# Kernel optimization log

Hardware: AMD Instinct MI355X
Metric: run time of the kernel (lower is better)

Reference implementation:

```python
import jax, jax.numpy as jnp
import numpy as np

HEADS = 16
DIM_HEAD = 64
SCALE = DIM_HEAD ** -0.5
LN_EPS = 1e-5


def setup_inputs() -> dict:
    key = jax.random.key(0)
    k1, k2, k3 = jax.random.split(key, 3)
    b, s, d = 2, 2048, 1024
    inner = HEADS * DIM_HEAD
    x = jax.random.normal(k1, (b, s, d), dtype=jnp.float32)
    w_qkv = jax.random.normal(k2, (d, 3 * inner), dtype=jnp.float32) * (d ** -0.5)
    w_out = jax.random.normal(k3, (inner, d), dtype=jnp.float32) * (inner ** -0.5)
    return {
        "x": x,
        "ln_gamma": jnp.ones((d,), jnp.float32),
        "ln_beta": jnp.zeros((d,), jnp.float32),
        "w_qkv": w_qkv,
        "w_out": w_out,
        "b_out": jnp.zeros((d,), jnp.float32),
    }


def _layernorm(x, gamma, beta):
    mu = jnp.mean(x, axis=-1, keepdims=True)
    var = jnp.var(x, axis=-1, keepdims=True)
    return (x - mu) * jax.lax.rsqrt(var + LN_EPS) * gamma + beta


def reference(x, ln_gamma, ln_beta, w_qkv, w_out, b_out):
    b, s, d = x.shape
    xn = _layernorm(x, ln_gamma, ln_beta)
    qkv = xn @ w_qkv                       # [b, s, 3*inner]
    q, k, v = jnp.split(qkv, 3, axis=-1)
    def heads(t):
        return t.reshape(b, s, HEADS, DIM_HEAD).transpose(0, 2, 1, 3)  # [b, h, s, dh]
    q, k, v = heads(q), heads(k), heads(v)
    dots = jnp.einsum("bhqd,bhkd->bhqk", q, k) * SCALE   # [b, h, s, s]
    attn = jax.nn.softmax(dots, axis=-1)
    out = jnp.einsum("bhqk,bhkd->bhqd", attn, v)          # [b, h, s, dh]
    out = out.transpose(0, 2, 1, 3).reshape(b, s, HEADS * DIM_HEAD)
    return out @ w_out + b_out
```

## Files before the change

kernel.cpp:

```cpp
#include <hip/hip_runtime.h>
#include <hip/hip_bf16.h>
#include <stdint.h>

#define NH     16
#define DHEAD  64
#define SEQ    2048
#define DMODEL 1024
#define NBATCH 2
#define INNER  1024
#define QKVN   3072
#define ROWS   4096
#define ATT_QB 64
#define ATT_KB 64

typedef __attribute__((ext_vector_type(8))) __bf16 bf16x8;
typedef __attribute__((ext_vector_type(4))) float floatx4;
typedef __attribute__((ext_vector_type(16))) float floatx16;

__device__ __forceinline__ unsigned short f2bf(float f) {
    union { __bf16 b; unsigned short u; } c; c.b = (__bf16)f; return c.u;
}

__device__ __forceinline__ unsigned int pk2(float lo, float hi) {
    union { ushort2 s; unsigned int u; } c;
    c.s.x = f2bf(lo); c.s.y = f2bf(hi); return c.u;
}

__device__ __forceinline__ float fexp2(float x) {
#if __has_builtin(__builtin_amdgcn_exp2f)
    return __builtin_amdgcn_exp2f(x);
#else
    float r; asm("v_exp_f32 %0, %1" : "=v"(r) : "v"(x)); return r;
#endif
}

typedef __attribute__((address_space(1))) void gvoid;
typedef __attribute__((address_space(3))) void lvoid;
__device__ __forceinline__ void gl_lds16(const void* g, void* l) {
    __builtin_amdgcn_global_load_lds((gvoid*)g, (lvoid*)l, 16, 0, 0);
}

__global__ __launch_bounds__(256) void prep_kernel(
        const float* __restrict__ x,
        const float* __restrict__ gamma,
        const float* __restrict__ beta,
        unsigned short* __restrict__ xn,
        const float* __restrict__ wqkv, unsigned short* __restrict__ wqkvT,
        const float* __restrict__ wout, unsigned short* __restrict__ woutT) {
    __shared__ unsigned short tile[32][33];
    __shared__ float red[4][2];
    const int t = threadIdx.x;
    if (blockIdx.z == 2) {
        const int row = blockIdx.y * 128 + blockIdx.x;
        const size_t base = (size_t)row * DMODEL + t * 4;
        float4 v = *(const float4*)(x + base);
        float s  = v.x + v.y + v.z + v.w;
        float ss = v.x*v.x + v.y*v.y + v.z*v.z + v.w*v.w;
        for (int off = 32; off >= 1; off >>= 1) {
            s  += __shfl_xor(s,  off);
            ss += __shfl_xor(ss, off);
        }
        const int w = t >> 6, lane = t & 63;
        if (lane == 0) { red[w][0] = s; red[w][1] = ss; }
        __syncthreads();
        if (t == 0) {
            float S  = red[0][0] + red[1][0] + red[2][0] + red[3][0];
            float SS = red[0][1] + red[1][1] + red[2][1] + red[3][1];
            float mu  = S * (1.f / DMODEL);
            float var = SS * (1.f / DMODEL) - mu * mu;
            red[0][0] = mu; red[0][1] = rsqrtf(var + 1e-5f);
        }
        __syncthreads();
        const float mu = red[0][0], rstd = red[0][1];
        float4 g = *(const float4*)(gamma + t * 4);
        float4 bb = *(const float4*)(beta + t * 4);
        ushort4 o;
        o.x = f2bf((v.x - mu) * rstd * g.x + bb.x);
        o.y = f2bf((v.y - mu) * rstd * g.y + bb.y);
        o.z = f2bf((v.z - mu) * rstd * g.z + bb.z);
        o.w = f2bf((v.w - mu) * rstd * g.w + bb.w);
        *(ushort4*)(xn + base) = o;
        return;
    }
    const float* in; unsigned short* out; int rows, cols;
    if (blockIdx.z == 0) {
        if (blockIdx.x >= QKVN / 32) return;
        in = wqkv; out = wqkvT; rows = DMODEL; cols = QKVN;
    } else {
        if (blockIdx.x >= DMODEL / 32) return;
        in = wout; out = woutT; rows = INNER; cols = DMODEL;
    }
    const int bx = blockIdx.x * 32, by = blockIdx.y * 32;
    const int tx = t & 31, ty = t >> 5;
    for (int i = ty; i < 32; i += 8)
        tile[i][tx] = f2bf(in[(size_t)(by + i) * cols + bx + tx]);
    __syncthreads();
    for (int i = ty; i < 32; i += 8)
        out[(size_t)(bx + i) * rows + by + tx] = tile[tx][i];
}

__global__ __launch_bounds__(256) void gemm_qkv(
        const unsigned short* __restrict__ A,
        const unsigned short* __restrict__ Bt,
        unsigned short* __restrict__ qP,
        unsigned short* __restrict__ kP,
        unsigned short* __restrict__ vT) {
    const int K = DMODEL;
    __shared__ __align__(16) unsigned short smem[3 * 8192];
    const int t = threadIdx.x;
    const int mBase = blockIdx.y * 128, nBase = blockIdx.x * 128;
    const int w = t >> 6, lane = t & 63, quad = lane >> 4, l16 = lane & 15;
    const int wm = (w >> 1) * 64, wn = (w & 1) * 64;
    const int srow = t >> 2, sch = t & 3;
    floatx4 acc[4][4];
    for (int mi = 0; mi < 4; mi++)
        for (int ni = 0; ni < 4; ni++) acc[mi][ni] = (floatx4)0.f;

    auto stage = [&](int k0, int bi) {
        unsigned short* sA = smem + bi * 8192;
        unsigned short* sB = sA + 4096;
        #pragma unroll
        for (int c = 0; c < 2; c++) {
            const int row = c * 64 + srow;
            const int gcol = (sch ^ ((row >> 1) & 3)) * 8;
            gl_lds16(&A[(size_t)(mBase + row) * K + k0 + gcol], &sA[(c * 256 + w * 64) * 8]);
            gl_lds16(&Bt[(size_t)(nBase + row) * K + k0 + gcol], &sB[(c * 256 + w * 64) * 8]);
        }
    };

    const int NK = K / 32;
    stage(0, 0);
    stage(32, 1);
    for (int kk = 0; kk < NK; ++kk) {
        if (kk + 1 < NK) { asm volatile("s_waitcnt vmcnt(4)" ::: "memory"); }
        else             { asm volatile("s_waitcnt vmcnt(0)" ::: "memory"); }
        __builtin_amdgcn_sched_barrier(0);
        __builtin_amdgcn_s_barrier();
        const unsigned short* sA = smem + (kk % 3) * 8192;
        const unsigned short* sB = sA + 4096;
        bf16x8 af[4], bfv[4];
        #pragma unroll
        for (int mi = 0; mi < 4; mi++) {
            const int r = wm + mi * 16 + l16;
            af[mi] = *(const bf16x8*)&sA[r * 32 + (quad ^ ((r >> 1) & 3)) * 8];
        }
        #pragma unroll
        for (int ni = 0; ni < 4; ni++) {
            const int r = wn + ni * 16 + l16;
            bfv[ni] = *(const bf16x8*)&sB[r * 32 + (quad ^ ((r >> 1) & 3)) * 8];
        }
        if (kk + 2 < NK) stage((kk + 2) * 32, (kk + 2) % 3);
        __builtin_amdgcn_s_setprio(1);
        #pragma unroll
        for (int mi = 0; mi < 4; mi++)
            #pragma unroll
            for (int ni = 0; ni < 4; ni++)
                acc[mi][ni] = __builtin_amdgcn_mfma_f32_16x16x32_bf16(
                    af[mi], bfv[ni], acc[mi][ni], 0, 0, 0);
        __builtin_amdgcn_s_setprio(0);
    }
    __syncthreads();
    const int reg = nBase >> 10;
    if (reg == 2) {
        #pragma unroll
        for (int ni = 0; ni < 4; ni++) {
            const int col = nBase + wn + ni * 16 + l16;
            const int h = (col & 1023) >> 6, dh = col & 63;
            #pragma unroll
            for (int mi = 0; mi < 4; mi++) {
                const int row0 = mBase + wm + mi * 16 + quad * 4;
                const int b = row0 >> 11, s0 = row0 & 2047;
                ushort4 o;
                o.x = f2bf(acc[mi][ni][0]); o.y = f2bf(acc[mi][ni][1]);
                o.z = f2bf(acc[mi][ni][2]); o.w = f2bf(acc[mi][ni][3]);
                *(ushort4*)&vT[((size_t)(b * NH + h) * DHEAD + dh) * SEQ + s0] = o;
            }
        }
    } else {
        unsigned short* dst = (reg == 0) ? qP : kP;
        const float scl = (reg == 0) ? 0.18033688011112042f : 1.f;
        const int hh = ((nBase + wn) & 1023) >> 6;
        unsigned short* tb_ = smem + w * (64 * 72);
        #pragma unroll
        for (int mi = 0; mi < 4; mi++)
            #pragma unroll
            for (int ni = 0; ni < 4; ni++)
                #pragma unroll
                for (int i = 0; i < 4; i++)
                    tb_[(mi * 16 + quad * 4 + i) * 72 + ni * 16 + l16] =
                        f2bf(acc[mi][ni][i] * scl);
        asm volatile("s_waitcnt lgkmcnt(0)" ::: "memory");
        const int row_g = mBase + wm + lane;
        const int b = row_g >> 11, sr = row_g & 2047;
        unsigned short* orow = dst + ((size_t)(b * NH + hh) * SEQ + sr) * DHEAD;
        #pragma unroll
        for (int c = 0; c < 8; c++)
            *(bf16x8*)&orow[c * 8] = *(const bf16x8*)&tb_[lane * 72 + c * 8];
    }
}

__global__ __launch_bounds__(256) void gemm_out(
        const unsigned short* __restrict__ A,
        const unsigned short* __restrict__ Bt,
        float* __restrict__ C,
        const int M, const int N, const int K,
        const float* __restrict__ bias) {
    __shared__ __align__(16) unsigned short smem[3 * 6144];
    const int t = threadIdx.x;
    const int mBase = blockIdx.y * 128, nBase = blockIdx.x * 64;
    const int w = t >> 6, lane = t & 63, quad = lane >> 4, l16 = lane & 15;
    const int wm = (w >> 1) * 64, wn = (w & 1) * 32;
    const int srow = t >> 2, sch = t & 3;
    floatx4 acc[4][2];
    for (int mi = 0; mi < 4; mi++)
        for (int ni = 0; ni < 2; ni++) acc[mi][ni] = (floatx4)0.f;

    auto stage = [&](int k0, int bi) {
        unsigned short* sA = smem + bi * 6144;
        unsigned short* sB = sA + 4096;
        #pragma unroll
        for (int c = 0; c < 2; c++) {
            const int row = c * 64 + srow;
            const int gcol = (sch ^ ((row >> 1) & 3)) * 8;
            gl_lds16(&A[(size_t)(mBase + row) * K + k0 + gcol], &sA[(c * 256 + w * 64) * 8]);
        }
        {
            const int gcol = (sch ^ ((srow >> 1) & 3)) * 8;
            gl_lds16(&Bt[(size_t)(nBase + srow) * K + k0 + gcol], &sB[(w * 64) * 8]);
        }
    };

    const int NK = K / 32;
    stage(0, 0);
    stage(32, 1);
    for (int kk = 0; kk < NK; ++kk) {
        if (kk + 1 < NK) { asm volatile("s_waitcnt vmcnt(3)" ::: "memory"); }
        else             { asm volatile("s_waitcnt vmcnt(0)" ::: "memory"); }
        __builtin_amdgcn_sched_barrier(0);
        __builtin_amdgcn_s_barrier();
        const unsigned short* sA = smem + (kk % 3) * 6144;
        const unsigned short* sB = sA + 4096;
        bf16x8 af[4], bfv[2];
        #pragma unroll
        for (int mi = 0; mi < 4; mi++) {
            const int r = wm + mi * 16 + l16;
            af[mi] = *(const bf16x8*)&sA[r * 32 + (quad ^ ((r >> 1) & 3)) * 8];
        }
        #pragma unroll
        for (int ni = 0; ni < 2; ni++) {
            const int r = wn + ni * 16 + l16;
            bfv[ni] = *(const bf16x8*)&sB[r * 32 + (quad ^ ((r >> 1) & 3)) * 8];
        }
        if (kk + 2 < NK) stage((kk + 2) * 32, (kk + 2) % 3);
        __builtin_amdgcn_s_setprio(1);
        #pragma unroll
        for (int mi = 0; mi < 4; mi++)
            #pragma unroll
            for (int ni = 0; ni < 2; ni++)
                acc[mi][ni] = __builtin_amdgcn_mfma_f32_16x16x32_bf16(
                    af[mi], bfv[ni], acc[mi][ni], 0, 0, 0);
        __builtin_amdgcn_s_setprio(0);
    }
    #pragma unroll
    for (int mi = 0; mi < 4; mi++)
        #pragma unroll
        for (int ni = 0; ni < 2; ni++) {
            const int col = nBase + wn + ni * 16 + l16;
            const float badd = bias ? bias[col] : 0.f;
            #pragma unroll
            for (int i = 0; i < 4; i++) {
                const int row = mBase + wm + mi * 16 + quad * 4 + i;
                C[(size_t)row * N + col] = acc[mi][ni][i] + badd;
            }
        }
}

__global__ __launch_bounds__(256, 4) void attn_kernel(
        const unsigned short* __restrict__ qP,
        const unsigned short* __restrict__ kP,
        const unsigned short* __restrict__ vT,
        unsigned short* __restrict__ aout) {
    __shared__ __align__(16) unsigned short sK[2][ATT_KB * 64];
    __shared__ __align__(16) unsigned short sV[2][ATT_KB * 64];
    const int t = threadIdx.x, w = t >> 6, lane = t & 63;
    const int l32 = lane & 31, half = lane >> 5;
    const int qh = w & 1, kh = w >> 1;
    const int bid = blockIdx.x;
    const int xcd = bid & 7, slot = bid >> 3;
    const int bh = xcd * 4 + (slot >> 5);
    const int qb = slot & 31;
    const int b = bh >> 4, h = bh & 15;
    const int qbase = qb * ATT_QB + qh * 32;

    bf16x8 qf[4];
    #pragma unroll
    for (int kd = 0; kd < 4; kd++)
        qf[kd] = *(const bf16x8*)&qP[
            ((size_t)bh * SEQ + qbase + l32) * DHEAD + kd * 16 + half * 8];

    floatx16 oac[2];
    oac[0] = (floatx16)0.f; oac[1] = (floatx16)0.f;
    float lS = 0.f;

    const unsigned short* kb = kP + (size_t)bh * SEQ * DHEAD;
    const unsigned short* vb = vT + (size_t)bh * DHEAD * SEQ;
    const int r8 = lane >> 3, sw8 = ((lane & 7) ^ r8) * 8;

    auto stage = [&](int it, int bi) {
        const int kv0 = it * ATT_KB;
        #pragma unroll
        for (int ii = 0; ii < 2; ii++) {
            const int row = w * 16 + ii * 8 + r8;
            gl_lds16(kb + (size_t)(kv0 + row) * DHEAD + sw8,
                     (void*)&sK[bi][(w * 16 + ii * 8) * 64]);
            gl_lds16(vb + (size_t)row * SEQ + kv0 + sw8,
                     (void*)&sV[bi][(w * 16 + ii * 8) * 64]);
        }
    };
    stage(0, 0);

    const int NIT = SEQ / ATT_KB;
    for (int it = 0; it < NIT; ++it) {
        __syncthreads();
        const int bi = it & 1;
        if (it + 1 < NIT) stage(it + 1, bi ^ 1);

        bf16x8 kf[4];
        #pragma unroll
        for (int kd = 0; kd < 4; kd++) {
            const int r = kh * 32 + l32;
            kf[kd] = *(const bf16x8*)&sK[bi][r * 64 + 8 * ((2 * kd + half) ^ (l32 & 7))];
        }

        floatx16 sv = (floatx16)0.f;
        __builtin_amdgcn_s_setprio(1);
        #pragma unroll
        for (int kd = 0; kd < 4; kd++)
            sv = __builtin_amdgcn_mfma_f32_32x32x16_bf16(kf[kd], qf[kd], sv, 0, 0, 0);
        __builtin_amdgcn_s_setprio(0);

        float p[16];
        #pragma unroll
        for (int i = 0; i < 16; i++) p[i] = fexp2(sv[i]);
        {
            float s = 0.f;
            #pragma unroll
            for (int i = 0; i < 16; i++) s += p[i];
            s += __shfl_xor(s, 32);
            lS += s;
        }

        bf16x8 pf[2];
        #pragma unroll
        for (int kd = 0; kd < 2; kd++) {
            const int base = kd * 8;
            unsigned int c01 = pk2(p[base + 0], p[base + 1]);
            unsigned int c23 = pk2(p[base + 2], p[base + 3]);
            unsigned int c45 = pk2(p[base + 4], p[base + 5]);
            unsigned int c67 = pk2(p[base + 6], p[base + 7]);
            asm("v_permlane32_swap_b32 %0, %1" : "+v"(c01), "+v"(c45));
            asm("v_permlane32_swap_b32 %0, %1" : "+v"(c23), "+v"(c67));
            union { unsigned int u[4]; bf16x8 v; } fr;
            fr.u[0] = c01; fr.u[1] = c23; fr.u[2] = c45; fr.u[3] = c67;
            pf[kd] = fr.v;
        }

        __builtin_amdgcn_s_setprio(1);
        #pragma unroll
        for (int dt = 0; dt < 2; dt++)
            #pragma unroll
            for (int kd = 0; kd < 2; kd++) {
                const int r = dt * 32 + l32;
                bf16x8 vf = *(const bf16x8*)&sV[bi][
                    r * 64 + 8 * ((kh * 4 + kd * 2 + half) ^ (l32 & 7))];
                oac[dt] = __builtin_amdgcn_mfma_f32_32x32x16_bf16(vf, pf[kd], oac[dt], 0, 0, 0);
            }
        __builtin_amdgcn_s_setprio(0);
    }

    __syncthreads();
    float* redO = (float*)&sK[0][0];
    float* redL = (float*)&sV[0][0];
    if (kh == 1) {
        #pragma unroll
        for (int dt = 0; dt < 2; dt++)
            #pragma unroll
            for (int g = 0; g < 4; g++) {
                const int c = dt * 4 + g;
                float4 o4;
                o4.x = oac[dt][g * 4 + 0]; o4.y = oac[dt][g * 4 + 1];
                o4.z = oac[dt][g * 4 + 2]; o4.w = oac[dt][g * 4 + 3];
                *(float4*)&redO[((size_t)qh * 64 + lane) * 32 + 4 * (c ^ (lane & 7))] = o4;
            }
        if (half == 0) redL[qh * 32 + l32] = lS;
    }
    __syncthreads();
    if (kh == 0) {
        #pragma unroll
        for (int dt = 0; dt < 2; dt++)
            #pragma unroll
            for (int g = 0; g < 4; g++) {
                const int c = dt * 4 + g;
                float4 o4 = *(const float4*)&redO[
                    ((size_t)qh * 64 + lane) * 32 + 4 * (c ^ (lane & 7))];
                oac[dt][g * 4 + 0] += o4.x; oac[dt][g * 4 + 1] += o4.y;
                oac[dt][g * 4 + 2] += o4.z; oac[dt][g * 4 + 3] += o4.w;
            }
        lS += redL[qh * 32 + l32];
        const float rl = 1.f / lS;
        unsigned short* orow = aout + ((size_t)(b * SEQ + qbase + l32)) * INNER + h * DHEAD;
        #pragma unroll
        for (int dt = 0; dt < 2; dt++)
            #pragma unroll
            for (int g = 0; g < 4; g++) {
                ushort4 o;
                o.x = f2bf(oac[dt][g * 4 + 0] * rl);
                o.y = f2bf(oac[dt][g * 4 + 1] * rl);
                o.z = f2bf(oac[dt][g * 4 + 2] * rl);
                o.w = f2bf(oac[dt][g * 4 + 3] * rl);
                *(ushort4*)&orow[dt * 32 + g * 8 + half * 4] = o;
            }
    }
}

extern "C" void kernel_launch(void* const* d_in, const int* in_sizes, int n_in,
                              void* d_out, int out_size, void* d_ws, size_t ws_size,
                              hipStream_t stream) {
    const float* x     = (const float*)d_in[0];
    const float* gamma = (const float*)d_in[1];
    const float* beta  = (const float*)d_in[2];
    const float* wqkv  = (const float*)d_in[3];
    const float* wout  = (const float*)d_in[4];
    const float* bout  = (const float*)d_in[5];
    float* out = (float*)d_out;

    unsigned short* ws     = (unsigned short*)d_ws;
    unsigned short* xn     = ws;
    unsigned short* wqkvT  = xn     + (size_t)ROWS * DMODEL;
    unsigned short* qPb    = wqkvT  + (size_t)QKVN * DMODEL;
    unsigned short* kPb    = qPb    + (size_t)NBATCH * NH * SEQ * DHEAD;
    unsigned short* vTb    = kPb    + (size_t)NBATCH * NH * SEQ * DHEAD;
    unsigned short* attnO  = vTb    + (size_t)NBATCH * NH * SEQ * DHEAD;
    unsigned short* woutT  = attnO  + (size_t)ROWS * INNER;

    prep_kernel<<<dim3(128, 32, 3), 256, 0, stream>>>(
        x, gamma, beta, xn, wqkv, wqkvT, wout, woutT);
    gemm_qkv<<<dim3(QKVN / 128, ROWS / 128), 256, 0, stream>>>(xn, wqkvT, qPb, kPb, vTb);
    attn_kernel<<<dim3((SEQ / ATT_QB) * NBATCH * NH), 256, 0, stream>>>(
        qPb, kPb, vTb, attnO);
    gemm_out<<<dim3(DMODEL / 64, ROWS / 128), 256, 0, stream>>>(
        attnO, woutT, out, ROWS, DMODEL, INNER, bout);
}
```

Before: 193.6 us.

## Double attention query block to 128 with 8-wave blocks sharing K/V tiles

The attention kernel now handles 128 query rows per block with 512 threads (8 waves: 4 query groups by 2 key halves), where it previously used 64 rows with 4 waves. Each staged K/V tile in LDS is therefore reused by twice as many query rows, which halves global K/V traffic and staging instructions per query. Each wave now issues one async load per matrix per stage. The grid halves to 512 blocks, which lowers the block count relative to CUs, and the reduction buffers are reorganized, with redL moved into its own shared array.

```diff
diff --git a/kernel.cpp b/kernel.cpp
--- a/kernel.cpp
+++ b/kernel.cpp
@@ -10,7 +10,7 @@
 #define INNER  1024
 #define QKVN   3072
 #define ROWS   4096
-#define ATT_QB 64
+#define ATT_QB 128
 #define ATT_KB 64
 
 typedef __attribute__((ext_vector_type(8))) __bf16 bf16x8;
@@ -275,22 +275,24 @@
         }
 }
 
-__global__ __launch_bounds__(256, 4) void attn_kernel(
+__global__ __launch_bounds__(512, 4) void attn_kernel(
         const unsigned short* __restrict__ qP,
         const unsigned short* __restrict__ kP,
         const unsigned short* __restrict__ vT,
         unsigned short* __restrict__ aout) {
-    __shared__ __align__(16) unsigned short sK[2][ATT_KB * 64];
-    __shared__ __align__(16) unsigned short sV[2][ATT_KB * 64];
+    __shared__ __align__(16) unsigned short kvs[16384];
+    __shared__ float redL[4][32];
+    unsigned short* sK0 = kvs;
+    unsigned short* sV0 = kvs + 8192;
     const int t = threadIdx.x, w = t >> 6, lane = t & 63;
     const int l32 = lane & 31, half = lane >> 5;
-    const int qh = w & 1, kh = w >> 1;
+    const int qq = w & 3, kh = w >> 2;
     const int bid = blockIdx.x;
     const int xcd = bid & 7, slot = bid >> 3;
-    const int bh = xcd * 4 + (slot >> 5);
-    const int qb = slot & 31;
+    const int bh = xcd * 4 + (slot >> 4);
+    const int qb = slot & 15;
     const int b = bh >> 4, h = bh & 15;
-    const int qbase = qb * ATT_QB + qh * 32;
+    const int qbase = qb * ATT_QB + qq * 32;
 
     bf16x8 qf[4];
     #pragma unroll
@@ -308,14 +310,11 @@
 
     auto stage = [&](int it, int bi) {
         const int kv0 = it * ATT_KB;
-        #pragma unroll
-        for (int ii = 0; ii < 2; ii++) {
-            const int row = w * 16 + ii * 8 + r8;
-            gl_lds16(kb + (size_t)(kv0 + row) * DHEAD + sw8,
-                     (void*)&sK[bi][(w * 16 + ii * 8) * 64]);
-            gl_lds16(vb + (size_t)row * SEQ + kv0 + sw8,
-                     (void*)&sV[bi][(w * 16 + ii * 8) * 64]);
-        }
+        const int row = w * 8 + r8;
+        gl_lds16(kb + (size_t)(kv0 + row) * DHEAD + sw8,
+                 (void*)&sK0[bi * 4096 + (w * 8) * 64]);
+        gl_lds16(vb + (size_t)row * SEQ + kv0 + sw8,
+                 (void*)&sV0[bi * 4096 + (w * 8) * 64]);
     };
     stage(0, 0);
 
@@ -329,7 +328,8 @@
         #pragma unroll
         for (int kd = 0; kd < 4; kd++) {
             const int r = kh * 32 + l32;
-            kf[kd] = *(const bf16x8*)&sK[bi][r * 64 + 8 * ((2 * kd + half) ^ (l32 & 7))];
+            kf[kd] = *(const bf16x8*)&sK0[bi * 4096 + r * 64 +
+                                          8 * ((2 * kd + half) ^ (l32 & 7))];
         }
 
         floatx16 sv = (floatx16)0.f;
@@ -371,16 +371,15 @@
             #pragma unroll
             for (int kd = 0; kd < 2; kd++) {
                 const int r = dt * 32 + l32;
-                bf16x8 vf = *(const bf16x8*)&sV[bi][
-                    r * 64 + 8 * ((kh * 4 + kd * 2 + half) ^ (l32 & 7))];
+                bf16x8 vf = *(const bf16x8*)&sV0[bi * 4096 + r * 64 +
+                    8 * ((kh * 4 + kd * 2 + half) ^ (l32 & 7))];
                 oac[dt] = __builtin_amdgcn_mfma_f32_32x32x16_bf16(vf, pf[kd], oac[dt], 0, 0, 0);
             }
         __builtin_amdgcn_s_setprio(0);
     }
 
     __syncthreads();
-    float* redO = (float*)&sK[0][0];
-    float* redL = (float*)&sV[0][0];
+    float* redO = (float*)kvs;
     if (kh == 1) {
         #pragma unroll
         for (int dt = 0; dt < 2; dt++)
@@ -390,9 +389,9 @@
                 float4 o4;
                 o4.x = oac[dt][g * 4 + 0]; o4.y = oac[dt][g * 4 + 1];
                 o4.z = oac[dt][g * 4 + 2]; o4.w = oac[dt][g * 4 + 3];
-                *(float4*)&redO[((size_t)qh * 64 + lane) * 32 + 4 * (c ^ (lane & 7))] = o4;
-            }
-        if (half == 0) redL[qh * 32 + l32] = lS;
+                *(float4*)&redO[((size_t)qq * 64 + lane) * 32 + 4 * (c ^ (lane & 7))] = o4;
+            }
+        if (half == 0) redL[qq][l32] = lS;
     }
     __syncthreads();
     if (kh == 0) {
@@ -402,11 +401,11 @@
             for (int g = 0; g < 4; g++) {
                 const int c = dt * 4 + g;
                 float4 o4 = *(const float4*)&redO[
-                    ((size_t)qh * 64 + lane) * 32 + 4 * (c ^ (lane & 7))];
+                    ((size_t)qq * 64 + lane) * 32 + 4 * (c ^ (lane & 7))];
                 oac[dt][g * 4 + 0] += o4.x; oac[dt][g * 4 + 1] += o4.y;
                 oac[dt][g * 4 + 2] += o4.z; oac[dt][g * 4 + 3] += o4.w;
             }
-        lS += redL[qh * 32 + l32];
+        lS += redL[qq][l32];
         const float rl = 1.f / lS;
         unsigned short* orow = aout + ((size_t)(b * SEQ + qbase + l32)) * INNER + h * DHEAD;
         #pragma unroll
@@ -446,7 +445,7 @@
     prep_kernel<<<dim3(128, 32, 3), 256, 0, stream>>>(
         x, gamma, beta, xn, wqkv, wqkvT, wout, woutT);
     gemm_qkv<<<dim3(QKVN / 128, ROWS / 128), 256, 0, stream>>>(xn, wqkvT, qPb, kPb, vTb);
-    attn_kernel<<<dim3((SEQ / ATT_QB) * NBATCH * NH), 256, 0, stream>>>(
+    attn_kernel<<<dim3((SEQ / ATT_QB) * NBATCH * NH), 512, 0, stream>>>(
         qPb, kPb, vTb, attnO);
     gemm_out<<<dim3(DMODEL / 64, ROWS / 128), 256, 0, stream>>>(
         attnO, woutT, out, ROWS, DMODEL, INNER, bout);
```

New measurement: 188.4 us. -2.7%, faster.
